# Performance work log

Measured on AMD Instinct MI355X. Metric: run time of the kernel, lower is better.

Reference implementation:

```python
import jax, jax.numpy as jnp
import numpy as np

N_VOCAB_TOTAL = 32064  # n_vocab + n_nts
D_MODEL = 256


def setup_inputs() -> dict:
    key = jax.random.key(0)
    ks = jax.random.split(key, 8)
    d = D_MODEL
    tokens = jax.random.randint(ks[0], (64, 4095), 0, N_VOCAB_TOTAL, dtype=jnp.int32)
    # embedding_tgt: normal with std 1/sqrt(d) (reset_parameters)
    E = jax.random.normal(ks[1], (N_VOCAB_TOTAL, d), dtype=jnp.float32) / jnp.sqrt(jnp.float32(d))
    s_in = 1.0 / np.sqrt(3 * d)
    s_h = 1.0 / np.sqrt(d)
    W_in = jax.random.uniform(ks[2], (d, 3 * d), jnp.float32, -s_in, s_in)  # Linear(3d, d)
    b_in = jax.random.uniform(ks[3], (d,), jnp.float32, -s_in, s_in)
    W1 = jax.random.uniform(ks[4], (d, d), jnp.float32, -s_h, s_h)
    b1 = jax.random.uniform(ks[5], (d,), jnp.float32, -s_h, s_h)
    W2 = jax.random.uniform(ks[6], (d, d), jnp.float32, -s_h, s_h)
    b2 = jax.random.uniform(ks[7], (d,), jnp.float32, -s_h, s_h)
    return {"tokens": tokens, "E": E, "W_in": W_in, "b_in": b_in,
            "W1": W1, "b1": b1, "W2": W2, "b2": b2}


def _bin_agg(roots, left, right, W_in, b_in, W1, b1, W2, b2):
    # skipmlp_binary_agg: root + hidden(inp(cat([root,left,right])))
    # hidden = ELU -> Linear -> ELU -> Linear  (nlayers=2)
    x = jnp.concatenate([roots, left, right], axis=-1)        # [..., 3d]
    h = x @ W_in.T + b_in                                     # inp: Linear(3d, d)
    h = jax.nn.elu(h) @ W1.T + b1
    h = jax.nn.elu(h) @ W2.T + b2
    return roots + h


def reference(tokens, E, W_in, b_in, W1, b1, W2, b2):
    # tokens: [B, N] heap-ordered perfect binary trees, N = 2^(D+1)-1.
    B, N = tokens.shape
    n_leaves = (N + 1) // 2
    emb = E[tokens]                                           # [B, N, d] gather
    cur = emb[:, N - n_leaves:]                               # leaf level, [B, 2^D, d]
    level = n_leaves // 2
    while level >= 1:                                          # fixed D iterations
        roots = emb[:, level - 1: 2 * level - 1]               # [B, level, d]
        left = cur[:, 0::2]
        right = cur[:, 1::2]
        cur = _bin_agg(roots, left, right, W_in, b_in, W1, b1, W2, b2)
        level //= 2
    return cur[:, 0]                                           # [B, d] root embeddings
```

## Files before the change

### kernel.cpp

```cpp
#include <hip/hip_runtime.h>
#include <stdint.h>


typedef __attribute__((ext_vector_type(8))) short short8;
typedef __attribute__((ext_vector_type(4))) float f32x4;

#define XS_STRIDE 264
#define TOK_N 4095

__device__ __forceinline__ unsigned short f32_to_bf16(float f) {
    union { float f; unsigned u; } v; v.f = f;
    return (unsigned short)((v.u + 0x7fffu + ((v.u >> 16) & 1u)) >> 16);
}
__device__ __forceinline__ float bf16_to_f32(unsigned short u) {
    union { unsigned u; float f; } v; v.u = ((unsigned)u) << 16; return v.f;
}

__global__ void convert_f32_bf16(const float* __restrict__ E,
                                 const float* __restrict__ Win,
                                 const float* __restrict__ W1,
                                 const float* __restrict__ W2,
                                 unsigned short* __restrict__ Ebf,
                                 unsigned short* __restrict__ Winbf,
                                 unsigned short* __restrict__ W1bf,
                                 unsigned short* __restrict__ W2bf) {
    const int nE = 32064 * 256, nWin = 256 * 768, nW = 256 * 256;
    const int total4 = (nE + nWin + 2 * nW) >> 2;
    for (int i = blockIdx.x * blockDim.x + threadIdx.x; i < total4;
         i += gridDim.x * blockDim.x) {
        int idx = i << 2;
        const float* src; unsigned short* dst; int off;
        if (idx < nE)                  { src = E;   dst = Ebf;   off = idx; }
        else if (idx < nE + nWin)      { src = Win; dst = Winbf; off = idx - nE; }
        else if (idx < nE + nWin + nW) { src = W1;  dst = W1bf;  off = idx - nE - nWin; }
        else                           { src = W2;  dst = W2bf;  off = idx - nE - nWin - nW; }
        float4 f = *(const float4*)(src + off);
        ushort4 o;
        o.x = f32_to_bf16(f.x); o.y = f32_to_bf16(f.y);
        o.z = f32_to_bf16(f.z); o.w = f32_to_bf16(f.w);
        *(ushort4*)(dst + off) = o;
    }
}

template<int MT>
__device__ __forceinline__ void acc_bias_init(f32x4 (&acc)[MT][4],
                                              const float* __restrict__ b,
                                              int n0, int l15) {
    float bv[4];
#pragma unroll
    for (int nt = 0; nt < 4; ++nt) bv[nt] = b[n0 + nt * 16 + l15];
#pragma unroll
    for (int mt = 0; mt < MT; ++mt)
#pragma unroll
        for (int nt = 0; nt < 4; ++nt)
            acc[mt][nt] = (f32x4){bv[nt], bv[nt], bv[nt], bv[nt]};
}

template<int MT>
__device__ __forceinline__ void mfma_gemm(const unsigned short* Xs,
                                          f32x4 (&acc)[MT][4],
                                          const unsigned short* __restrict__ base,
                                          int nstride, int kbase,
                                          int l15, int q) {
    short8 bb[2][4];
#pragma unroll
    for (int k = 0; k < 2; ++k)
#pragma unroll
        for (int nt = 0; nt < 4; ++nt)
            bb[k][nt] = *(const short8*)(base + (size_t)(nt * 16) * nstride + kbase + k * 32);
#pragma unroll
    for (int k = 0; k < 8; ++k) {
        short8 a[MT];
#pragma unroll
        for (int mt = 0; mt < MT; ++mt)
            a[mt] = *(const short8*)(&Xs[(mt * 16 + l15) * XS_STRIDE + k * 32 + q * 8]);
#pragma unroll
        for (int mt = 0; mt < MT; ++mt)
#pragma unroll
            for (int nt = 0; nt < 4; ++nt)
                acc[mt][nt] = __builtin_amdgcn_mfma_f32_16x16x32_bf16(
                    a[mt], bb[k & 1][nt], acc[mt][nt], 0, 0, 0);
        if (k + 2 < 8) {
#pragma unroll
            for (int nt = 0; nt < 4; ++nt)
                bb[k & 1][nt] = *(const short8*)(base + (size_t)(nt * 16) * nstride + kbase + (k + 2) * 32);
        }
    }
}

template<int MT>
__device__ __forceinline__ void mfma_gemm_deep(const unsigned short* Xs,
                                               f32x4 (&acc)[MT][4],
                                               const unsigned short* __restrict__ base,
                                               int nstride, int kbase,
                                               int l15, int q) {
#pragma unroll
    for (int h = 0; h < 2; ++h) {
        short8 bb[4][4];
#pragma unroll
        for (int k = 0; k < 4; ++k)
#pragma unroll
            for (int nt = 0; nt < 4; ++nt)
                bb[k][nt] = *(const short8*)(base + (size_t)(nt * 16) * nstride
                                             + kbase + (h * 4 + k) * 32);
#pragma unroll
        for (int k = 0; k < 4; ++k) {
            short8 a[MT];
#pragma unroll
            for (int mt = 0; mt < MT; ++mt)
                a[mt] = *(const short8*)(&Xs[(mt * 16 + l15) * XS_STRIDE
                                             + (h * 4 + k) * 32 + q * 8]);
#pragma unroll
            for (int mt = 0; mt < MT; ++mt)
#pragma unroll
                for (int nt = 0; nt < 4; ++nt)
                    acc[mt][nt] = __builtin_amdgcn_mfma_f32_16x16x32_bf16(
                        a[mt], bb[k][nt], acc[mt][nt], 0, 0, 0);
        }
    }
}

template<int MT>
__device__ __forceinline__ void elu_store_Xs(unsigned short* Xs,
                                             f32x4 (&acc)[MT][4],
                                             int n0, int l15, int q) {
#pragma unroll
    for (int mt = 0; mt < MT; ++mt)
#pragma unroll
        for (int nt = 0; nt < 4; ++nt)
#pragma unroll
            for (int r = 0; r < 4; ++r) {
                float h = acc[mt][nt][r];
                h = h > 0.f ? h : (__expf(h) - 1.f);
                Xs[(mt * 16 + q * 4 + r) * XS_STRIDE + n0 + nt * 16 + l15] = f32_to_bf16(h);
            }
}

template<int MT>
__global__ __launch_bounds__(256, (MT == 8) ? 2 : 4)
void tree_level(const int* __restrict__ tokens,
                const unsigned short* __restrict__ Ebf,
                const unsigned short* __restrict__ Win,
                const unsigned short* __restrict__ W1,
                const unsigned short* __restrict__ W2,
                const float* __restrict__ b_in,
                const float* __restrict__ b1,
                const float* __restrict__ b2,
                const unsigned short* __restrict__ cur_in,
                unsigned short* __restrict__ cur_out,
                int L, int logL, int first)
{
    constexpr int R = MT * 16;
    constexpr int GITER = R / 8;
    constexpr bool PF = (MT < 8);
    extern __shared__ unsigned short Xs[];

    const int tid  = threadIdx.x;
    const int lane = tid & 63;
    const int wid  = tid >> 6;
    const int l15  = lane & 15;
    const int q    = lane >> 4;
    const int n0   = wid * 64;
    const int blk  = blockIdx.x;
    const int c    = tid & 31;
    const int sub  = tid >> 5;

    auto gsrc = [&](int p, int r) -> const unsigned short* {
        int g = blk * R + r;
        int b = g >> logL;
        int i = g - (b << logL);
        if (p == 0) {
            int tok = tokens[b * TOK_N + (L - 1) + i];
            return Ebf + (size_t)tok * 256;
        } else if (first) {
            int tok = tokens[b * TOK_N + 2047 + 2 * i + (p - 1)];
            return Ebf + (size_t)tok * 256;
        } else {
            return cur_in + ((size_t)b * (2 * L) + 2 * i + (p - 1)) * 256;
        }
    };

    auto stage = [&](int p) {
        short8 t[GITER];
#pragma unroll
        for (int it = 0; it < GITER; ++it)
            t[it] = *(const short8*)(gsrc(p, it * 8 + sub) + c * 8);
#pragma unroll
        for (int it = 0; it < GITER; ++it)
            *(short8*)(&Xs[(it * 8 + sub) * XS_STRIDE + c * 8]) = t[it];
    };

    f32x4 acc[MT][4];
    short8 g[PF ? GITER : 1];

    if constexpr (PF) {
#pragma unroll
        for (int it = 0; it < GITER; ++it)
            g[it] = *(const short8*)(gsrc(0, it * 8 + sub) + c * 8);
#pragma unroll
        for (int it = 0; it < GITER; ++it)
            *(short8*)(&Xs[(it * 8 + sub) * XS_STRIDE + c * 8]) = g[it];
    } else {
        stage(0);
    }
    __syncthreads();

    acc_bias_init<MT>(acc, b_in, n0, l15);
    const unsigned short* wbase = Win + q * 8 + (size_t)(n0 + l15) * 768;
    for (int p = 0; p < 3; ++p) {
        if constexpr (PF) {
            if (p < 2) {
#pragma unroll
                for (int it = 0; it < GITER; ++it)
                    g[it] = *(const short8*)(gsrc(p + 1, it * 8 + sub) + c * 8);
            }
        }
        mfma_gemm<MT>(Xs, acc, wbase, 768, p * 256, l15, q);
        __syncthreads();
        if (p < 2) {
            if constexpr (PF) {
#pragma unroll
                for (int it = 0; it < GITER; ++it)
                    *(short8*)(&Xs[(it * 8 + sub) * XS_STRIDE + c * 8]) = g[it];
            } else {
                stage(p + 1);
            }
            __syncthreads();
        }
    }

    elu_store_Xs<MT>(Xs, acc, n0, l15, q);
    __syncthreads();

    acc_bias_init<MT>(acc, b1, n0, l15);
    if constexpr (PF) {
#pragma unroll
        for (int it = 0; it < GITER; ++it)
            g[it] = *(const short8*)(gsrc(0, it * 8 + sub) + c * 8);
    }
    mfma_gemm<MT>(Xs, acc, W1 + q * 8 + (size_t)(n0 + l15) * 256, 256, 0, l15, q);
    __syncthreads();

    elu_store_Xs<MT>(Xs, acc, n0, l15, q);
    __syncthreads();

    acc_bias_init<MT>(acc, b2, n0, l15);
    mfma_gemm<MT>(Xs, acc, W2 + q * 8 + (size_t)(n0 + l15) * 256, 256, 0, l15, q);
    __syncthreads();
    if constexpr (PF) {
#pragma unroll
        for (int it = 0; it < GITER; ++it)
            *(short8*)(&Xs[(it * 8 + sub) * XS_STRIDE + c * 8]) = g[it];
    } else {
        stage(0);
    }
    __syncthreads();

#pragma unroll
    for (int mt = 0; mt < MT; ++mt)
#pragma unroll
        for (int r = 0; r < 4; ++r) {
            int row = mt * 16 + q * 4 + r;
#pragma unroll
            for (int nt = 0; nt < 4; ++nt) {
                int col = n0 + nt * 16 + l15;
                float o = acc[mt][nt][r] + bf16_to_f32(Xs[row * XS_STRIDE + col]);
                Xs[row * XS_STRIDE + col] = f32_to_bf16(o);
            }
        }
    __syncthreads();
#pragma unroll
    for (int it = 0; it < GITER; ++it) {
        int row = it * 8 + sub;
        *(short8*)(cur_out + ((size_t)(blk * R + row)) * 256 + c * 8) =
            *(const short8*)(&Xs[row * XS_STRIDE + c * 8]);
    }
}

__device__ __attribute__((noinline)) void tail_level_rt(
    const int* __restrict__ tokens,
    const unsigned short* __restrict__ Ebf,
    const unsigned short* __restrict__ Win,
    const unsigned short* __restrict__ W1,
    const unsigned short* __restrict__ W2,
    const float* __restrict__ b_in,
    const float* __restrict__ b1,
    const float* __restrict__ b2,
    const unsigned short* __restrict__ cur_in,
    float* __restrict__ final_out,
    int b, int n0, int l15, int q, int c, int sub,
    int L, int first_lvl, int last_lvl)
{
    constexpr int MT = 2;
    __shared__ unsigned short Xs[32 * XS_STRIDE];
    __shared__ unsigned short Pv[32 * 256];

    const int Lm = L - 1;

    short8 gr[4];
    auto ld_root = [&]() {
#pragma unroll
        for (int it = 0; it < 4; ++it) {
            int row = it * 8 + sub;
            int il  = row & Lm;
            int tok = tokens[b * TOK_N + Lm + il];
            gr[it] = *(const short8*)(Ebf + (size_t)tok * 256 + c * 8);
        }
    };
    auto park_root = [&]() {
#pragma unroll
        for (int it = 0; it < 4; ++it)
            *(short8*)(&Xs[(it * 8 + sub) * XS_STRIDE + c * 8]) = gr[it];
    };
    auto stg_lr = [&](int p) {
        if (first_lvl) {
            short8 t[4];
#pragma unroll
            for (int it = 0; it < 4; ++it) {
                int row = it * 8 + sub;
                int il  = row & Lm;
                t[it] = *(const short8*)(cur_in + ((size_t)b * (2 * L) + 2 * il + (p - 1)) * 256 + c * 8);
            }
#pragma unroll
            for (int it = 0; it < 4; ++it)
                *(short8*)(&Xs[(it * 8 + sub) * XS_STRIDE + c * 8]) = t[it];
        } else {
#pragma unroll
            for (int it = 0; it < 4; ++it) {
                int row = it * 8 + sub;
                int il  = row & Lm;
                short8 t = *(const short8*)(&Pv[(2 * il + (p - 1)) * 256 + c * 8]);
                *(short8*)(&Xs[row * XS_STRIDE + c * 8]) = t;
            }
        }
    };

    f32x4 acc[MT][4];

    ld_root();
    park_root();
    __syncthreads();

    acc_bias_init<MT>(acc, b_in, n0, l15);
    const unsigned short* wbase = Win + q * 8 + (size_t)(n0 + l15) * 768;
#pragma unroll 1
    for (int p = 0; p < 3; ++p) {
        mfma_gemm_deep<MT>(Xs, acc, wbase, 768, p * 256, l15, q);
        __syncthreads();
        if (p < 2) { stg_lr(p + 1); __syncthreads(); }
    }

    elu_store_Xs<MT>(Xs, acc, n0, l15, q);
    __syncthreads();

    acc_bias_init<MT>(acc, b1, n0, l15);
    mfma_gemm_deep<MT>(Xs, acc, W1 + q * 8 + (size_t)(n0 + l15) * 256, 256, 0, l15, q);
    __syncthreads();

    elu_store_Xs<MT>(Xs, acc, n0, l15, q);
    __syncthreads();

    acc_bias_init<MT>(acc, b2, n0, l15);
    mfma_gemm_deep<MT>(Xs, acc, W2 + q * 8 + (size_t)(n0 + l15) * 256, 256, 0, l15, q);
    __syncthreads();
    park_root();
    __syncthreads();

    if (last_lvl) {
#pragma unroll
        for (int mt = 0; mt < MT; ++mt)
#pragma unroll
            for (int r = 0; r < 4; ++r) {
                int row = mt * 16 + q * 4 + r;
                if (row == 0) {
#pragma unroll
                    for (int nt = 0; nt < 4; ++nt) {
                        int col = n0 + nt * 16 + l15;
                        final_out[(size_t)b * 256 + col] =
                            acc[mt][nt][r] + bf16_to_f32(Xs[row * XS_STRIDE + col]);
                    }
                }
            }
    } else {
#pragma unroll
        for (int mt = 0; mt < MT; ++mt)
#pragma unroll
            for (int r = 0; r < 4; ++r) {
                int row = mt * 16 + q * 4 + r;
                if (row < L) {
#pragma unroll
                    for (int nt = 0; nt < 4; ++nt) {
                        int col = n0 + nt * 16 + l15;
                        float o = acc[mt][nt][r] + bf16_to_f32(Xs[row * XS_STRIDE + col]);
                        Pv[row * 256 + col] = f32_to_bf16(o);
                    }
                }
            }
    }
    __syncthreads();
}

__global__ __launch_bounds__(256, 2)
void tree_tail32(const int* __restrict__ tokens,
                 const unsigned short* __restrict__ Ebf,
                 const unsigned short* __restrict__ Win,
                 const unsigned short* __restrict__ W1,
                 const unsigned short* __restrict__ W2,
                 const float* __restrict__ b_in,
                 const float* __restrict__ b1,
                 const float* __restrict__ b2,
                 const unsigned short* __restrict__ cur_in,
                 float* __restrict__ final_out)
{
    const int tid  = threadIdx.x;
    const int lane = tid & 63;
    const int wid  = tid >> 6;
    const int l15  = lane & 15;
    const int q    = lane >> 4;
    const int n0   = wid * 64;
    const int b    = blockIdx.x;
    const int c    = tid & 31;
    const int sub  = tid >> 5;

#pragma unroll 1
    for (int L = 32; L >= 1; L >>= 1) {
        tail_level_rt(tokens, Ebf, Win, W1, W2, b_in, b1, b2,
                      cur_in, final_out, b, n0, l15, q, c, sub,
                      L, L == 32, L == 1);
    }
}

extern "C" void kernel_launch(void* const* d_in, const int* in_sizes, int n_in,
                              void* d_out, int out_size, void* d_ws, size_t ws_size,
                              hipStream_t stream) {
    const int*   tokens = (const int*)  d_in[0];
    const float* E      = (const float*)d_in[1];
    const float* W_in   = (const float*)d_in[2];
    const float* b_in   = (const float*)d_in[3];
    const float* W1     = (const float*)d_in[4];
    const float* b1     = (const float*)d_in[5];
    const float* W2     = (const float*)d_in[6];
    const float* b2     = (const float*)d_in[7];
    float* out = (float*)d_out;
    char* ws = (char*)d_ws;

    unsigned short* Ebf   = (unsigned short*)(ws);
    unsigned short* Winbf = (unsigned short*)(ws + 16416768);
    unsigned short* W1bf  = (unsigned short*)(ws + 16809984);
    unsigned short* W2bf  = (unsigned short*)(ws + 16941056);
    unsigned short* curA  = (unsigned short*)(ws + 17072128);
    unsigned short* curB  = (unsigned short*)(ws + 50626560);

    static bool attr_done = false;
    if (!attr_done) {
        void (*k8)(const int*, const unsigned short*, const unsigned short*,
                   const unsigned short*, const unsigned short*, const float*,
                   const float*, const float*, const unsigned short*,
                   unsigned short*, int, int, int) = tree_level<8>;
        (void)hipFuncSetAttribute(reinterpret_cast<const void*>(k8),
                                  hipFuncAttributeMaxDynamicSharedMemorySize,
                                  128 * XS_STRIDE * 2);
        attr_done = true;
    }

    convert_f32_bf16<<<1024, 256, 0, stream>>>(E, W_in, W1, W2,
                                               Ebf, Winbf, W1bf, W2bf);

    tree_level<8><<<dim3(512), dim3(256), 128 * XS_STRIDE * 2, stream>>>(
        tokens, Ebf, Winbf, W1bf, W2bf, b_in, b1, b2,
        nullptr, curA, 1024, 10, 1);
    tree_level<8><<<dim3(256), dim3(256), 128 * XS_STRIDE * 2, stream>>>(
        tokens, Ebf, Winbf, W1bf, W2bf, b_in, b1, b2,
        curA, curB, 512, 9, 0);
    tree_level<2><<<dim3(512), dim3(256), 32 * XS_STRIDE * 2, stream>>>(
        tokens, Ebf, Winbf, W1bf, W2bf, b_in, b1, b2,
        curB, curA, 256, 8, 0);
    tree_level<1><<<dim3(512), dim3(256), 16 * XS_STRIDE * 2, stream>>>(
        tokens, Ebf, Winbf, W1bf, W2bf, b_in, b1, b2,
        curA, curB, 128, 7, 0);
    tree_level<1><<<dim3(256), dim3(256), 16 * XS_STRIDE * 2, stream>>>(
        tokens, Ebf, Winbf, W1bf, W2bf, b_in, b1, b2,
        curB, curA, 64, 6, 0);
    tree_tail32<<<dim3(64), dim3(256), 0, stream>>>(
        tokens, Ebf, Winbf, W1bf, W2bf, b_in, b1, b2, curA, out);
}
```

Before: 482.2 us.

## Preload all tail-level roots and children into LDS, unroll tail levels at compile time

The tail kernel now loads all 63 root embeddings and the 64 child vectors into LDS once at the start. It stores children in even/odd slots so the left and right operands are contiguous 32-row blocks, and runs the first-layer GEMM directly from those LDS regions with no staging copies or barriers between the three K-chunks. The per-level noinline runtime loop becomes compile-time templated levels, which removes repeated root gathers and several syncs per level. The cost is about 84 KB of dynamic LDS per block, fine here since the tail runs only 64 blocks.

```diff
diff --git a/kernel.cpp b/kernel.cpp
--- a/kernel.cpp
+++ b/kernel.cpp
@@ -89,11 +89,11 @@
 }
 
 template<int MT>
-__device__ __forceinline__ void mfma_gemm_deep(const unsigned short* Xs,
-                                               f32x4 (&acc)[MT][4],
-                                               const unsigned short* __restrict__ base,
-                                               int nstride, int kbase,
-                                               int l15, int q) {
+__device__ __forceinline__ void gemm_lds(const unsigned short* A,
+                                         f32x4 (&acc)[MT][4],
+                                         const unsigned short* __restrict__ wb,
+                                         int nstride, int kbase,
+                                         int l15, int q) {
 #pragma unroll
     for (int h = 0; h < 2; ++h) {
         short8 bb[4][4];
@@ -101,15 +101,15 @@
         for (int k = 0; k < 4; ++k)
 #pragma unroll
             for (int nt = 0; nt < 4; ++nt)
-                bb[k][nt] = *(const short8*)(base + (size_t)(nt * 16) * nstride
+                bb[k][nt] = *(const short8*)(wb + (size_t)(nt * 16) * nstride
                                              + kbase + (h * 4 + k) * 32);
 #pragma unroll
         for (int k = 0; k < 4; ++k) {
             short8 a[MT];
 #pragma unroll
             for (int mt = 0; mt < MT; ++mt)
-                a[mt] = *(const short8*)(&Xs[(mt * 16 + l15) * XS_STRIDE
-                                             + (h * 4 + k) * 32 + q * 8]);
+                a[mt] = *(const short8*)(&A[(mt * 16 + l15) * XS_STRIDE
+                                            + (h * 4 + k) * 32 + q * 8]);
 #pragma unroll
             for (int mt = 0; mt < MT; ++mt)
 #pragma unroll
@@ -277,96 +277,41 @@
     }
 }
 
-__device__ __attribute__((noinline)) void tail_level_rt(
-    const int* __restrict__ tokens,
-    const unsigned short* __restrict__ Ebf,
+template<int L, bool LAST>
+__device__ __forceinline__ void tail_lvl(
     const unsigned short* __restrict__ Win,
     const unsigned short* __restrict__ W1,
     const unsigned short* __restrict__ W2,
     const float* __restrict__ b_in,
     const float* __restrict__ b1,
     const float* __restrict__ b2,
-    const unsigned short* __restrict__ cur_in,
     float* __restrict__ final_out,
-    int b, int n0, int l15, int q, int c, int sub,
-    int L, int first_lvl, int last_lvl)
+    unsigned short* Xs, unsigned short* Pv, const unsigned short* Rt,
+    int b, int n0, int l15, int q)
 {
     constexpr int MT = 2;
-    __shared__ unsigned short Xs[32 * XS_STRIDE];
-    __shared__ unsigned short Pv[32 * 256];
-
-    const int Lm = L - 1;
-
-    short8 gr[4];
-    auto ld_root = [&]() {
-#pragma unroll
-        for (int it = 0; it < 4; ++it) {
-            int row = it * 8 + sub;
-            int il  = row & Lm;
-            int tok = tokens[b * TOK_N + Lm + il];
-            gr[it] = *(const short8*)(Ebf + (size_t)tok * 256 + c * 8);
-        }
-    };
-    auto park_root = [&]() {
-#pragma unroll
-        for (int it = 0; it < 4; ++it)
-            *(short8*)(&Xs[(it * 8 + sub) * XS_STRIDE + c * 8]) = gr[it];
-    };
-    auto stg_lr = [&](int p) {
-        if (first_lvl) {
-            short8 t[4];
-#pragma unroll
-            for (int it = 0; it < 4; ++it) {
-                int row = it * 8 + sub;
-                int il  = row & Lm;
-                t[it] = *(const short8*)(cur_in + ((size_t)b * (2 * L) + 2 * il + (p - 1)) * 256 + c * 8);
-            }
-#pragma unroll
-            for (int it = 0; it < 4; ++it)
-                *(short8*)(&Xs[(it * 8 + sub) * XS_STRIDE + c * 8]) = t[it];
-        } else {
-#pragma unroll
-            for (int it = 0; it < 4; ++it) {
-                int row = it * 8 + sub;
-                int il  = row & Lm;
-                short8 t = *(const short8*)(&Pv[(2 * il + (p - 1)) * 256 + c * 8]);
-                *(short8*)(&Xs[row * XS_STRIDE + c * 8]) = t;
-            }
-        }
-    };
-
     f32x4 acc[MT][4];
-
-    ld_root();
-    park_root();
-    __syncthreads();
 
     acc_bias_init<MT>(acc, b_in, n0, l15);
     const unsigned short* wbase = Win + q * 8 + (size_t)(n0 + l15) * 768;
-#pragma unroll 1
-    for (int p = 0; p < 3; ++p) {
-        mfma_gemm_deep<MT>(Xs, acc, wbase, 768, p * 256, l15, q);
-        __syncthreads();
-        if (p < 2) { stg_lr(p + 1); __syncthreads(); }
-    }
+    gemm_lds<MT>(Rt + (L - 1) * XS_STRIDE, acc, wbase, 768, 0,   l15, q);
+    gemm_lds<MT>(Pv,                       acc, wbase, 768, 256, l15, q);
+    gemm_lds<MT>(Pv + 32 * XS_STRIDE,      acc, wbase, 768, 512, l15, q);
 
     elu_store_Xs<MT>(Xs, acc, n0, l15, q);
     __syncthreads();
 
     acc_bias_init<MT>(acc, b1, n0, l15);
-    mfma_gemm_deep<MT>(Xs, acc, W1 + q * 8 + (size_t)(n0 + l15) * 256, 256, 0, l15, q);
+    gemm_lds<MT>(Xs, acc, W1 + q * 8 + (size_t)(n0 + l15) * 256, 256, 0, l15, q);
     __syncthreads();
 
     elu_store_Xs<MT>(Xs, acc, n0, l15, q);
     __syncthreads();
 
     acc_bias_init<MT>(acc, b2, n0, l15);
-    mfma_gemm_deep<MT>(Xs, acc, W2 + q * 8 + (size_t)(n0 + l15) * 256, 256, 0, l15, q);
-    __syncthreads();
-    park_root();
-    __syncthreads();
-
-    if (last_lvl) {
+    gemm_lds<MT>(Xs, acc, W2 + q * 8 + (size_t)(n0 + l15) * 256, 256, 0, l15, q);
+
+    if constexpr (LAST) {
 #pragma unroll
         for (int mt = 0; mt < MT; ++mt)
 #pragma unroll
@@ -377,7 +322,7 @@
                     for (int nt = 0; nt < 4; ++nt) {
                         int col = n0 + nt * 16 + l15;
                         final_out[(size_t)b * 256 + col] =
-                            acc[mt][nt][r] + bf16_to_f32(Xs[row * XS_STRIDE + col]);
+                            acc[mt][nt][r] + bf16_to_f32(Rt[(L - 1) * XS_STRIDE + col]);
                     }
                 }
             }
@@ -388,11 +333,13 @@
             for (int r = 0; r < 4; ++r) {
                 int row = mt * 16 + q * 4 + r;
                 if (row < L) {
+                    int slot = (row >> 1) + (row & 1) * 32;
 #pragma unroll
                     for (int nt = 0; nt < 4; ++nt) {
                         int col = n0 + nt * 16 + l15;
-                        float o = acc[mt][nt][r] + bf16_to_f32(Xs[row * XS_STRIDE + col]);
-                        Pv[row * 256 + col] = f32_to_bf16(o);
+                        float o = acc[mt][nt][r]
+                                + bf16_to_f32(Rt[(L - 1 + row) * XS_STRIDE + col]);
+                        Pv[slot * XS_STRIDE + col] = f32_to_bf16(o);
                     }
                 }
             }
@@ -412,6 +359,11 @@
                  const unsigned short* __restrict__ cur_in,
                  float* __restrict__ final_out)
 {
+    extern __shared__ unsigned short lds[];
+    unsigned short* Xs = lds;
+    unsigned short* Pv = lds + 32 * XS_STRIDE;
+    unsigned short* Rt = lds + 96 * XS_STRIDE;
+
     const int tid  = threadIdx.x;
     const int lane = tid & 63;
     const int wid  = tid >> 6;
@@ -422,12 +374,42 @@
     const int c    = tid & 31;
     const int sub  = tid >> 5;
 
-#pragma unroll 1
-    for (int L = 32; L >= 1; L >>= 1) {
-        tail_level_rt(tokens, Ebf, Win, W1, W2, b_in, b1, b2,
-                      cur_in, final_out, b, n0, l15, q, c, sub,
-                      L, L == 32, L == 1);
-    }
+    {
+        short8 tp[8], tr[8];
+#pragma unroll
+        for (int it = 0; it < 8; ++it) {
+            int r = it * 8 + sub;
+            tp[it] = *(const short8*)(cur_in + ((size_t)b * 64 + r) * 256 + c * 8);
+        }
+#pragma unroll
+        for (int it = 0; it < 8; ++it) {
+            int r = it * 8 + sub;
+            if (r < 63) {
+                int tok = tokens[b * TOK_N + r];
+                tr[it] = *(const short8*)(Ebf + (size_t)tok * 256 + c * 8);
+            }
+        }
+#pragma unroll
+        for (int it = 0; it < 8; ++it) {
+            int r = it * 8 + sub;
+            int slot = (r >> 1) + (r & 1) * 32;
+            *(short8*)(&Pv[slot * XS_STRIDE + c * 8]) = tp[it];
+        }
+#pragma unroll
+        for (int it = 0; it < 8; ++it) {
+            int r = it * 8 + sub;
+            if (r < 63)
+                *(short8*)(&Rt[r * XS_STRIDE + c * 8]) = tr[it];
+        }
+    }
+    __syncthreads();
+
+    tail_lvl<32, false>(Win, W1, W2, b_in, b1, b2, final_out, Xs, Pv, Rt, b, n0, l15, q);
+    tail_lvl<16, false>(Win, W1, W2, b_in, b1, b2, final_out, Xs, Pv, Rt, b, n0, l15, q);
+    tail_lvl<8,  false>(Win, W1, W2, b_in, b1, b2, final_out, Xs, Pv, Rt, b, n0, l15, q);
+    tail_lvl<4,  false>(Win, W1, W2, b_in, b1, b2, final_out, Xs, Pv, Rt, b, n0, l15, q);
+    tail_lvl<2,  false>(Win, W1, W2, b_in, b1, b2, final_out, Xs, Pv, Rt, b, n0, l15, q);
+    tail_lvl<1,  true >(Win, W1, W2, b_in, b1, b2, final_out, Xs, Pv, Rt, b, n0, l15, q);
 }
 
 extern "C" void kernel_launch(void* const* d_in, const int* in_sizes, int n_in,
@@ -451,6 +433,8 @@
     unsigned short* curA  = (unsigned short*)(ws + 17072128);
     unsigned short* curB  = (unsigned short*)(ws + 50626560);
 
+    const int TAIL_LDS = 160 * XS_STRIDE * 2;
+
     static bool attr_done = false;
     if (!attr_done) {
         void (*k8)(const int*, const unsigned short*, const unsigned short*,
@@ -460,6 +444,9 @@
         (void)hipFuncSetAttribute(reinterpret_cast<const void*>(k8),
                                   hipFuncAttributeMaxDynamicSharedMemorySize,
                                   128 * XS_STRIDE * 2);
+        (void)hipFuncSetAttribute(reinterpret_cast<const void*>(&tree_tail32),
+                                  hipFuncAttributeMaxDynamicSharedMemorySize,
+                                  TAIL_LDS);
         attr_done = true;
     }
 
@@ -481,6 +468,6 @@
     tree_level<1><<<dim3(256), dim3(256), 16 * XS_STRIDE * 2, stream>>>(
         tokens, Ebf, Winbf, W1bf, W2bf, b_in, b1, b2,
         curB, curA, 64, 6, 0);
-    tree_tail32<<<dim3(64), dim3(256), 0, stream>>>(
+    tree_tail32<<<dim3(64), dim3(256), TAIL_LDS, stream>>>(
         tokens, Ebf, Winbf, W1bf, W2bf, b_in, b1, b2, curA, out);
 }
```

Result: no change. 479.7 us (-0.5%).
